# Kernel tuning notes

Measured on AMD Instinct MI355X. Metric: run time of the kernel, lower is better.

Reference implementation:

```python
import jax, jax.numpy as jnp
import numpy as np

T, B, NN = 20, 4, 500            # timesteps, batch, nodes per sample
M = B * NN                        # big-batched node count = 2000
IN_D, H, H2, OUT = 2, 128, 64, 32


def setup_inputs() -> dict:
    key = jax.random.key(0)
    ks = jax.random.split(key, 16)
    positions = jax.random.normal(ks[0], (T, M, IN_D), jnp.float32)
    adjacency = (jax.random.uniform(ks[1], (T, M, M)) < 0.01).astype(jnp.float32)
    adjacency = adjacency * (1.0 - jnp.eye(M, dtype=jnp.float32))
    ego_mask = jax.random.bernoulli(ks[2], 0.8, (B, T, NN))
    s = lambda k, shp, fan: (jax.random.normal(k, shp, jnp.float32) / np.sqrt(fan)).astype(jnp.float32)
    return {
        'positions': positions,
        'adjacency': adjacency,
        'ego_mask': ego_mask,
        'W1': s(ks[3], (IN_D, H), IN_D), 'b1': jnp.zeros((H,), jnp.float32),
        'W2': s(ks[4], (H, H), H),       'b2': jnp.zeros((H,), jnp.float32),
        'W_ih': s(ks[5], (4 * H, H), H), 'W_hh': s(ks[6], (4 * H, H), H),
        'b_ih': jnp.zeros((4 * H,), jnp.float32), 'b_hh': jnp.zeros((4 * H,), jnp.float32),
        'fc1_w': s(ks[7], (H, H2), H),   'fc1_b': jnp.zeros((H2,), jnp.float32),
        'fc2_w': s(ks[8], (H2, OUT), H2), 'fc2_b': jnp.zeros((OUT,), jnp.float32),
    }


def _forward(positions, adjacency, ego_mask, W1, b1, W2, b2,
             W_ih, W_hh, b_ih, b_hh, fc1_w, fc1_b, fc2_w, fc2_b):
    # ego_mask [B,T,NN] -> [T, B*NN] (matches permute(1,0,2).reshape(T,-1))
    mask = jnp.transpose(ego_mask, (1, 0, 2)).reshape(T, M).astype(positions.dtype)

    def gcn_timestep(x_t, a_t, m_t):
        # masked subgraph + self loops on kept nodes (PyG GCNConv normalization)
        Ahat = a_t * m_t[:, None] * m_t[None, :] + jnp.diag(m_t)   # [M,M]
        deg = Ahat.sum(axis=0)                                      # in-degree (col sum)
        dinv = jnp.where(deg > 0, jax.lax.rsqrt(jnp.maximum(deg, 1e-12)), 0.0)
        An = dinv[:, None] * Ahat * dinv[None, :]                   # D^-1/2 Ahat D^-1/2
        h1 = jax.nn.relu(An.T @ (x_t @ W1) + b1)                    # GCN1 + relu
        h2 = (An.T @ (h1 @ W2) + b2) * m_t[:, None]                 # GCN2, scatter into zeros
        return h2

    placeholder = jax.vmap(gcn_timestep)(positions, adjacency, mask)  # [T, M, H]

    # torch nn.LSTM (batch_first=False) on placeholder.transpose(0,1):
    # sequence axis = nodes (M), batch axis = T
    xs = jnp.transpose(placeholder, (1, 0, 2))  # [M, T, H]

    def lstm_step(carry, x_s):
        h, c = carry
        gates = x_s @ W_ih.T + b_ih + h @ W_hh.T + b_hh
        i, f, g, o = jnp.split(gates, 4, axis=-1)
        c = jax.nn.sigmoid(f) * c + jax.nn.sigmoid(i) * jnp.tanh(g)
        h = jax.nn.sigmoid(o) * jnp.tanh(c)
        return (h, c), h

    init = (jnp.zeros((T, H), positions.dtype), jnp.zeros((T, H), positions.dtype))
    _, lstm_out = jax.lax.scan(lstm_step, init, xs)  # [M, T, H]

    emb = lstm_out.reshape(B, NN, T, H)              # view(B, max_nodes, T, H)
    emb = jax.nn.relu(emb @ fc1_w + fc1_b)
    return emb @ fc2_w + fc2_b                       # [B, NN, T, OUT]


def reference(positions, adjacency, ego_mask, W1, b1, W2, b2,
              W_ih, W_hh, b_ih, b_hh, fc1_w, fc1_b, fc2_w, fc2_b):
    return _forward(positions, adjacency, ego_mask, W1, b1, W2, b2,
                    W_ih, W_hh, b_ih, b_hh, fc1_w, fc1_b, fc2_w, fc2_b)
```

## Files before the change

### kernel.cpp

```cpp
#include <hip/hip_runtime.h>
#include <hip/hip_bf16.h>

#define T_   20
#define B_   4
#define NN_  500
#define M_   2000
#define TM_  40000
#define H_   128
#define G_   512
#define H2_  64
#define OUT_ 32
#define ECAP 64
#define TG_  (T_ * G_)

typedef unsigned short ushort_t;
typedef unsigned int   uint_t;
typedef _Float16       f16;
typedef f16 f16x2 __attribute__((ext_vector_type(2)));

#if defined(__has_builtin)
#  if __has_builtin(__builtin_amdgcn_fdot2)
#    define HAVE_FDOT2 1
#  endif
#endif

__device__ inline float fdot2_(f16x2 a, f16x2 b, float c) {
#ifdef HAVE_FDOT2
    return __builtin_amdgcn_fdot2(a, b, c, false);
#else
    return c + (float)a.x * (float)b.x + (float)a.y * (float)b.y;
#endif
}

__device__ inline float fast_sig(float x) {
    float e = __builtin_amdgcn_exp2f(x * -1.4426950408889634f);
    return __builtin_amdgcn_rcpf(1.f + e);
}
__device__ inline float fast_tanh(float x) {
    float e = __builtin_amdgcn_exp2f(x * 2.8853900817779268f);
    return 1.f - 2.f * __builtin_amdgcn_rcpf(e + 1.f);
}

#define BARRAW() asm volatile("s_barrier" ::: "memory")

__global__ __launch_bounds__(1024) void k0_mask(const void* __restrict__ ego,
                                                float* __restrict__ mf,
                                                int* __restrict__ ecnt) {
    __shared__ int fl[3];
    int tid = threadIdx.x;
    if (tid < 3) fl[tid] = 0;
    __syncthreads();
    const uint_t* dw = (const uint_t*)ego;
    int a = 0, b = 0, c = 0;
    for (int i = tid; i < 2500; i += 1024) {
        uint_t v = dw[i];
        bool isf32  = (v == 0x3F800000u);
        bool isbf16 = (v == 0x00003F80u) || (v == 0x3F803F80u);
        if (isf32)  a = 1;
        if (isbf16) b = 1;
        if (v > 1u && !isf32 && !isbf16) c = 1;
    }
    if (a) fl[0] = 1;
    if (b) fl[1] = 1;
    if (c) fl[2] = 1;
    __syncthreads();
    int mode;
    if (fl[1])      mode = 3;
    else if (fl[0]) mode = 2;
    else if (fl[2]) mode = 1;
    else            mode = 0;
    int e = blockIdx.x * 1024 + tid;
    if (e >= TM_) return;
    ecnt[e] = 0;
    int t = e / M_, i = e % M_;
    int bb = i / NN_, n = i % NN_;
    int src = (bb * T_ + t) * NN_ + n;
    bool on;
    if (mode == 0)      on = ((const int*)ego)[src] != 0;
    else if (mode == 1) on = ((const unsigned char*)ego)[src] != 0;
    else if (mode == 2) on = ((const float*)ego)[src] != 0.f;
    else                on = ((const ushort_t*)ego)[src] != 0;
    mf[e] = on ? 1.f : 0.f;
}

#define JSTRIP 400
__global__ void k1_scan(const float* __restrict__ adj, const float* __restrict__ mf,
                        int* __restrict__ ecnt, int* __restrict__ edges) {
    __shared__ float ms[JSTRIP];
    int t = blockIdx.y, j0 = blockIdx.z * JSTRIP;
    int i = blockIdx.x * 256 + threadIdx.x;
    for (int idx = threadIdx.x; idx < JSTRIP; idx += 256)
        ms[idx] = mf[t * M_ + j0 + idx];
    __syncthreads();
    if (i >= M_) return;
    if (mf[t * M_ + i] == 0.f) return;
    const float* ap = adj + (size_t)t * M_ * M_ + (size_t)j0 * M_ + i;
    int r = t * M_ + i;
    int* ep = edges + (size_t)r * ECAP;
#pragma unroll 8
    for (int jj = 0; jj < JSTRIP; ++jj) {
        float av = ap[(size_t)jj * M_];
        if (av != 0.f && ms[jj] != 0.f) {
            int pos = atomicAdd(&ecnt[r], 1);
            if (pos < ECAP) ep[pos] = j0 + jj;
        }
    }
}

__global__ void k2_y1(const float* __restrict__ pos, const float* __restrict__ W1,
                      const float* __restrict__ mf, const int* __restrict__ ecnt,
                      float* __restrict__ dinv, f16* __restrict__ Y1) {
    int gid = blockIdx.x * 256 + threadIdx.x;
    int r = gid >> 7, h = gid & 127;
    if (r >= TM_) return;
    float mr = mf[r];
    int cnt = ecnt[r];
    float dv = (mr != 0.f) ? __frsqrt_rn((float)(cnt + 1)) : 0.f;
    if (h == 0) dinv[r] = dv;
    float2 xy = ((const float2*)pos)[r];
    float v = xy.x * W1[h] + xy.y * W1[H_ + h];
    Y1[gid] = (f16)(dv * v);
}

__global__ __launch_bounds__(64) void k3_agg1(const f16* __restrict__ Y1,
        const float* __restrict__ dinv, const int* __restrict__ ecnt,
        const int* __restrict__ edges, const float* __restrict__ b1,
        f16* __restrict__ h1) {
    int r = blockIdx.x, q = threadIdx.x;
    int t = r / M_, base = t * M_;
    const uint_t* Yu = (const uint_t*)Y1;
    f16x2 sp = __builtin_bit_cast(f16x2, Yu[(size_t)r * 64 + q]);
    float a0 = (float)sp.x, a1 = (float)sp.y;
    int ec = ecnt[r]; if (ec > ECAP) ec = ECAP;
    const int4* ep4 = (const int4*)(edges + (size_t)r * ECAP);
    for (int e = 0; e < ec; e += 4) {
        int4 ix = ep4[e >> 2];
        int j1 = (e + 1 < ec) ? ix.y : ix.x;
        int j2 = (e + 2 < ec) ? ix.z : ix.x;
        int j3 = (e + 3 < ec) ? ix.w : ix.x;
        uint_t u0 = Yu[(size_t)(base + ix.x) * 64 + q];
        uint_t u1 = Yu[(size_t)(base + j1) * 64 + q];
        uint_t u2 = Yu[(size_t)(base + j2) * 64 + q];
        uint_t u3 = Yu[(size_t)(base + j3) * 64 + q];
        f16x2 p0 = __builtin_bit_cast(f16x2, u0);
        a0 += (float)p0.x; a1 += (float)p0.y;
        if (e + 1 < ec) { f16x2 p = __builtin_bit_cast(f16x2, u1); a0 += (float)p.x; a1 += (float)p.y; }
        if (e + 2 < ec) { f16x2 p = __builtin_bit_cast(f16x2, u2); a0 += (float)p.x; a1 += (float)p.y; }
        if (e + 3 < ec) { f16x2 p = __builtin_bit_cast(f16x2, u3); a0 += (float)p.x; a1 += (float)p.y; }
    }
    float dv = dinv[r];
    float o0 = dv * a0 + b1[2 * q];
    float o1 = dv * a1 + b1[2 * q + 1];
    f16x2 op; op.x = (f16)fmaxf(o0, 0.f); op.y = (f16)fmaxf(o1, 0.f);
    ((uint_t*)h1)[(size_t)r * 64 + q] = __builtin_bit_cast(uint_t, op);
}

__global__ __launch_bounds__(64) void k5_agg2(const f16* __restrict__ Y2,
        const float* __restrict__ dinv, const float* __restrict__ mf,
        const int* __restrict__ ecnt, const int* __restrict__ edges,
        const float* __restrict__ b2, f16* __restrict__ ph) {
    int r = blockIdx.x, q = threadIdx.x;
    int t = r / M_, base = t * M_;
    const uint_t* Yu = (const uint_t*)Y2;
    f16x2 sp = __builtin_bit_cast(f16x2, Yu[(size_t)r * 64 + q]);
    float a0 = (float)sp.x, a1 = (float)sp.y;
    int ec = ecnt[r]; if (ec > ECAP) ec = ECAP;
    const int4* ep4 = (const int4*)(edges + (size_t)r * ECAP);
    for (int e = 0; e < ec; e += 4) {
        int4 ix = ep4[e >> 2];
        int j1 = (e + 1 < ec) ? ix.y : ix.x;
        int j2 = (e + 2 < ec) ? ix.z : ix.x;
        int j3 = (e + 3 < ec) ? ix.w : ix.x;
        uint_t u0 = Yu[(size_t)(base + ix.x) * 64 + q];
        uint_t u1 = Yu[(size_t)(base + j1) * 64 + q];
        uint_t u2 = Yu[(size_t)(base + j2) * 64 + q];
        uint_t u3 = Yu[(size_t)(base + j3) * 64 + q];
        f16x2 p0 = __builtin_bit_cast(f16x2, u0);
        a0 += (float)p0.x; a1 += (float)p0.y;
        if (e + 1 < ec) { f16x2 p = __builtin_bit_cast(f16x2, u1); a0 += (float)p.x; a1 += (float)p.y; }
        if (e + 2 < ec) { f16x2 p = __builtin_bit_cast(f16x2, u2); a0 += (float)p.x; a1 += (float)p.y; }
        if (e + 3 < ec) { f16x2 p = __builtin_bit_cast(f16x2, u3); a0 += (float)p.x; a1 += (float)p.y; }
    }
    float dv = dinv[r], mr = mf[r];
    f16x2 op;
    op.x = (f16)((dv * a0 + b2[2 * q]) * mr);
    op.y = (f16)((dv * a1 + b2[2 * q + 1]) * mr);
    ((uint_t*)ph)[(size_t)r * 64 + q] = __builtin_bit_cast(uint_t, op);
}

#define BM 32
#define BN 64
#define BLD (BN + 4)
__global__ __launch_bounds__(256) void kgemm(const f16* __restrict__ A,
        const float* __restrict__ Bw, int bTrans, int Ntot, int mode,
        const float* __restrict__ dinv, const float* __restrict__ ba,
        const float* __restrict__ bb, f16* __restrict__ Out) {
    __shared__ float As[H_ * BM];
    __shared__ float Bs[H_ * BLD];
    int m0 = blockIdx.x * BM;
    int nb = blockIdx.y;
    int tid = threadIdx.x;
    {
        int r = tid >> 3, kc = tid & 7;
        const f16* aprow = A + (size_t)(m0 + r) * H_ + kc * 16;
        float4 raw0 = ((const float4*)aprow)[0];
        float4 raw1 = ((const float4*)aprow)[1];
        f16 tmp[16];
        *(float4*)(tmp) = raw0;
        *(float4*)(tmp + 8) = raw1;
#pragma unroll
        for (int u = 0; u < 16; ++u) As[(kc * 16 + u) * BM + r] = (float)tmp[u];
    }
    if (bTrans == 0) {
        for (int idx = tid; idx < H_ * BN; idx += 256) {
            int k = idx >> 6, nl = idx & 63;
            Bs[k * BLD + nl] = Bw[k * Ntot + nb * BN + nl];
        }
    } else {
        for (int idx = tid; idx < H_ * BN; idx += 256) {
            int nl = idx >> 7, k = idx & 127;
            Bs[k * BLD + nl] = Bw[(size_t)(nb * BN + nl) * H_ + k];
        }
    }
    __syncthreads();
    int ty = tid >> 4, tx = tid & 15;
    float acc[2][4] = {};
#pragma unroll 4
    for (int k = 0; k < H_; ++k) {
        float2 a2 = *(const float2*)&As[k * BM + ty * 2];
        float4 b4 = *(const float4*)&Bs[k * BLD + tx * 4];
        acc[0][0] += a2.x * b4.x; acc[0][1] += a2.x * b4.y;
        acc[0][2] += a2.x * b4.z; acc[0][3] += a2.x * b4.w;
        acc[1][0] += a2.y * b4.x; acc[1][1] += a2.y * b4.y;
        acc[1][2] += a2.y * b4.z; acc[1][3] += a2.y * b4.w;
    }
#pragma unroll
    for (int rr = 0; rr < 2; ++rr) {
        int r = m0 + ty * 2 + rr;
        if (mode == 0) {
            float sc = dinv[r];
#pragma unroll
            for (int cc = 0; cc < 4; ++cc) {
                int n = nb * BN + tx * 4 + cc;
                Out[(size_t)r * Ntot + n] = (f16)(sc * acc[rr][cc]);
            }
        } else {
            int t = r / M_, s = r % M_;
#pragma unroll
            for (int cc = 0; cc < 4; ++cc) {
                int n = nb * BN + tx * 4 + cc;
                Out[((size_t)s * T_ + t) * G_ + n] =
                    (f16)(acc[rr][cc] + ba[n] + bb[n]);
            }
        }
    }
}

__global__ __launch_bounds__(512, 2) void k7_lstm(const float* __restrict__ Whh,
        const f16* __restrict__ xg, f16* __restrict__ lo) {
    __shared__ uint_t hbuf[H_ / 2];
    __shared__ float g4[G_];
    int t = blockIdx.x, j = threadIdx.x;
    f16x2 w[64];
    {
        const float* wr = Whh + (size_t)j * H_;
#pragma unroll
        for (int d = 0; d < 64; ++d) {
            f16x2 p;
            p.x = (f16)wr[2 * d];
            p.y = (f16)wr[2 * d + 1];
            w[d] = p;
        }
    }
    if (j < H_ / 2) hbuf[j] = 0;
    float cst = 0.f;
    const ushort_t* xpu = (const ushort_t*)xg + t * G_ + j;
    ushort_t xa[8], xb[8];
#pragma unroll
    for (int k = 0; k < 8; ++k) xa[k] = xpu[(size_t)k * TG_];
    __syncthreads();

#define LSTM_STEP(S, XV)                                                      \
    do {                                                                      \
        float acc = 0.f;                                                      \
        const uint4* hb = (const uint4*)hbuf;                                 \
        _Pragma("unroll")                                                     \
        for (int d = 0; d < 16; ++d) {                                        \
            uint4 hv = hb[d];                                                 \
            acc = fdot2_(w[4 * d + 0], __builtin_bit_cast(f16x2, hv.x), acc); \
            acc = fdot2_(w[4 * d + 1], __builtin_bit_cast(f16x2, hv.y), acc); \
            acc = fdot2_(w[4 * d + 2], __builtin_bit_cast(f16x2, hv.z), acc); \
            acc = fdot2_(w[4 * d + 3], __builtin_bit_cast(f16x2, hv.w), acc); \
        }                                                                     \
        acc += (float)__builtin_bit_cast(f16, (ushort_t)(XV));                \
        g4[j] = ((j >> 7) == 2) ? fast_tanh(acc) : fast_sig(acc);             \
        BARRAW();                                                             \
        if (j < H_) {                                                         \
            float si = g4[j], sf = g4[H_ + j];                                \
            float tg = g4[2 * H_ + j], so = g4[3 * H_ + j];                   \
            cst = sf * cst + si * tg;                                         \
            float h = so * fast_tanh(cst);                                    \
            f16 hh = (f16)h;                                                  \
            ((ushort_t*)hbuf)[j] = __builtin_bit_cast(ushort_t, hh);          \
            lo[((size_t)(S) * T_ + t) * H_ + j] = hh;                         \
        }                                                                     \
        BARRAW();                                                             \
    } while (0)

    for (int c2 = 0; c2 < 125; ++c2) {
        int sA = c2 * 16;
#pragma unroll
        for (int k = 0; k < 8; ++k) xb[k] = xpu[(size_t)(sA + 8 + k) * TG_];
#pragma unroll
        for (int k = 0; k < 8; ++k) LSTM_STEP(sA + k, xa[k]);
        int nbs = (sA + 16 <= TM_ / T_ - 8) ? sA + 16 : TM_ / T_ - 8;
#pragma unroll
        for (int k = 0; k < 8; ++k) xa[k] = xpu[(size_t)(nbs + k) * TG_];
#pragma unroll
        for (int k = 0; k < 8; ++k) LSTM_STEP(sA + 8 + k, xb[k]);
    }
#undef LSTM_STEP
}

__global__ __launch_bounds__(256) void k8_fc(const f16* __restrict__ lo,
        const float* __restrict__ w1, const float* __restrict__ fb1,
        const float* __restrict__ w2, const float* __restrict__ fb2,
        float* __restrict__ out) {
    __shared__ uint_t hl[4][H_ / 2];
    __shared__ float o1f[4][H2_];
    int tid = threadIdx.x;
    int o = tid & 63, rr = tid >> 6;
    f16x2 w1c[64];
#pragma unroll
    for (int d = 0; d < 64; ++d) {
        f16x2 p;
        p.x = (f16)w1[(2 * d) * H2_ + o];
        p.y = (f16)w1[(2 * d + 1) * H2_ + o];
        w1c[d] = p;
    }
    int o2 = o & 31;
    float w2f[64];
#pragma unroll
    for (int d = 0; d < 64; ++d) w2f[d] = w2[d * OUT_ + o2];
    float fb1v = fb1[o], fb2v = fb2[o2];

    for (int r0 = blockIdx.x * 4; r0 < TM_; r0 += 512 * 4) {
        {
            int row = tid >> 6, q = tid & 63;
            hl[row][q] = ((const uint_t*)lo)[(size_t)(r0 + row) * 64 + q];
        }
        __syncthreads();
        float acc = fb1v;
        const uint4* hb = (const uint4*)&hl[rr][0];
#pragma unroll
        for (int d = 0; d < 16; ++d) {
            uint4 hv = hb[d];
            acc = fdot2_(w1c[4 * d + 0], __builtin_bit_cast(f16x2, hv.x), acc);
            acc = fdot2_(w1c[4 * d + 1], __builtin_bit_cast(f16x2, hv.y), acc);
            acc = fdot2_(w1c[4 * d + 2], __builtin_bit_cast(f16x2, hv.z), acc);
            acc = fdot2_(w1c[4 * d + 3], __builtin_bit_cast(f16x2, hv.w), acc);
        }
        o1f[rr][o] = fmaxf(acc, 0.f);
        __syncthreads();
        if (o < OUT_) {
            float a2 = fb2v;
            const float4* ob = (const float4*)&o1f[rr][0];
#pragma unroll
            for (int d = 0; d < 16; ++d) {
                float4 v = ob[d];
                a2 += v.x * w2f[4 * d + 0] + v.y * w2f[4 * d + 1]
                    + v.z * w2f[4 * d + 2] + v.w * w2f[4 * d + 3];
            }
            out[(size_t)(r0 + rr) * OUT_ + o] = a2;
        }
        __syncthreads();
    }
}

extern "C" void kernel_launch(void* const* d_in, const int* in_sizes, int n_in,
                              void* d_out, int out_size, void* d_ws, size_t ws_size,
                              hipStream_t stream) {
    const float* positions = (const float*)d_in[0];
    const float* adjacency = (const float*)d_in[1];
    const void*  ego       = d_in[2];
    const float* W1   = (const float*)d_in[3];
    const float* b1   = (const float*)d_in[4];
    const float* W2   = (const float*)d_in[5];
    const float* b2   = (const float*)d_in[6];
    const float* W_ih = (const float*)d_in[7];
    const float* W_hh = (const float*)d_in[8];
    const float* b_ih = (const float*)d_in[9];
    const float* b_hh = (const float*)d_in[10];
    const float* fc1w = (const float*)d_in[11];
    const float* fc1b = (const float*)d_in[12];
    const float* fc2w = (const float*)d_in[13];
    const float* fc2b = (const float*)d_in[14];
    float* out = (float*)d_out;

    char* p = (char*)d_ws;
    auto alloc = [&](size_t bytes) {
        void* r = (void*)p;
        p += (bytes + 255) & ~(size_t)255;
        return r;
    };
    float* mf    = (float*)alloc((size_t)TM_ * 4);
    float* dinv  = (float*)alloc((size_t)TM_ * 4);
    int*   ecnt  = (int*)alloc((size_t)TM_ * 4);
    int*   edges = (int*)alloc((size_t)TM_ * ECAP * 4);
    f16*   bufC  = (f16*)alloc((size_t)TM_ * H_ * 2);
    f16*   bufD  = (f16*)alloc((size_t)TM_ * H_ * 2);
    f16*   xg    = (f16*)alloc((size_t)TM_ * G_ * 2);
    f16*   Y1 = bufC, *Y2 = bufC;
    f16*   h1 = bufD, *ph = bufD;
    f16*   lo = (f16*)edges;

    hipLaunchKernelGGL(k0_mask, dim3(40), dim3(1024), 0, stream, ego, mf, ecnt);
    hipLaunchKernelGGL(k1_scan, dim3(8, 20, 5), dim3(256), 0, stream,
                       adjacency, mf, ecnt, edges);
    hipLaunchKernelGGL(k2_y1, dim3(20000), dim3(256), 0, stream,
                       positions, W1, mf, ecnt, dinv, Y1);
    hipLaunchKernelGGL(k3_agg1, dim3(40000), dim3(64), 0, stream,
                       Y1, dinv, ecnt, edges, b1, h1);
    hipLaunchKernelGGL(kgemm, dim3(1250, 2), dim3(256), 0, stream,
                       h1, W2, 0, 128, 0, dinv, (const float*)nullptr,
                       (const float*)nullptr, Y2);
    hipLaunchKernelGGL(k5_agg2, dim3(40000), dim3(64), 0, stream,
                       Y2, dinv, mf, ecnt, edges, b2, ph);
    hipLaunchKernelGGL(kgemm, dim3(1250, 8), dim3(256), 0, stream,
                       ph, W_ih, 1, 512, 1, dinv, b_ih, b_hh, xg);
    hipLaunchKernelGGL(k7_lstm, dim3(20), dim3(512), 0, stream, W_hh, xg, lo);
    hipLaunchKernelGGL(k8_fc, dim3(512), dim3(256), 0, stream,
                       lo, fc1w, fc1b, fc2w, fc2b, out);
}
```

Before: 1.914 ms.

## Use MFMA for dense GEMMs, restructure LSTM step, and split adjacency scan finer

The fp32 FMA GEMM is replaced by an f16 MFMA kernel with 64x64 tiles in LDS. The LSTM kernel is reorganised so each group of four threads computes all four gates for one hidden unit, reduced with lane shuffles. This removes the gate shared-memory array and one barrier per step, and double-buffers the hidden state. The adjacency scan strip is halved to launch more blocks. The LSTM is a long serial chain, so cutting its per-step barriers and latency is likely the main target. The shuffle reductions add latency to each step in exchange.

Result: no change. 1.918 ms (+0.2%).

```diff
diff --git a/kernel.cpp b/kernel.cpp
--- a/kernel.cpp
+++ b/kernel.cpp
@@ -17,6 +17,8 @@
 typedef unsigned int   uint_t;
 typedef _Float16       f16;
 typedef f16 f16x2 __attribute__((ext_vector_type(2)));
+typedef f16 f16x8 __attribute__((ext_vector_type(8)));
+typedef float f32x4 __attribute__((ext_vector_type(4)));
 
 #if defined(__has_builtin)
 #  if __has_builtin(__builtin_amdgcn_fdot2)
@@ -83,7 +85,7 @@
     mf[e] = on ? 1.f : 0.f;
 }
 
-#define JSTRIP 400
+#define JSTRIP 200
 __global__ void k1_scan(const float* __restrict__ adj, const float* __restrict__ mf,
                         int* __restrict__ ecnt, int* __restrict__ edges) {
     __shared__ float ms[JSTRIP];
@@ -188,69 +190,80 @@
     ((uint_t*)ph)[(size_t)r * 64 + q] = __builtin_bit_cast(uint_t, op);
 }
 
-#define BM 32
-#define BN 64
-#define BLD (BN + 4)
-__global__ __launch_bounds__(256) void kgemm(const f16* __restrict__ A,
+#define ALD 136
+__global__ __launch_bounds__(256) void kgemm_mfma(const f16* __restrict__ A,
         const float* __restrict__ Bw, int bTrans, int Ntot, int mode,
         const float* __restrict__ dinv, const float* __restrict__ ba,
         const float* __restrict__ bb, f16* __restrict__ Out) {
-    __shared__ float As[H_ * BM];
-    __shared__ float Bs[H_ * BLD];
-    int m0 = blockIdx.x * BM;
-    int nb = blockIdx.y;
+    __shared__ f16 As[64 * ALD];
+    __shared__ f16 Bs[64 * ALD];
+    int m0 = blockIdx.x * 64;
+    int n0 = blockIdx.y * 64;
     int tid = threadIdx.x;
-    {
-        int r = tid >> 3, kc = tid & 7;
-        const f16* aprow = A + (size_t)(m0 + r) * H_ + kc * 16;
-        float4 raw0 = ((const float4*)aprow)[0];
-        float4 raw1 = ((const float4*)aprow)[1];
-        f16 tmp[16];
-        *(float4*)(tmp) = raw0;
-        *(float4*)(tmp + 8) = raw1;
-#pragma unroll
-        for (int u = 0; u < 16; ++u) As[(kc * 16 + u) * BM + r] = (float)tmp[u];
-    }
-    if (bTrans == 0) {
-        for (int idx = tid; idx < H_ * BN; idx += 256) {
-            int k = idx >> 6, nl = idx & 63;
-            Bs[k * BLD + nl] = Bw[k * Ntot + nb * BN + nl];
+#pragma unroll
+    for (int u = 0; u < 4; ++u) {
+        int idx = u * 256 + tid;
+        int row = idx >> 4, seg = idx & 15;
+        *(f16x8*)&As[row * ALD + seg * 8] =
+            *(const f16x8*)(A + (size_t)(m0 + row) * H_ + seg * 8);
+    }
+    if (bTrans) {
+#pragma unroll
+        for (int u = 0; u < 16; ++u) {
+            int idx = u * 256 + tid;
+            int n = idx >> 6, k2 = (idx & 63) * 2;
+            float2 v = *(const float2*)(Bw + (size_t)(n0 + n) * H_ + k2);
+            f16x2 pk; pk.x = (f16)v.x; pk.y = (f16)v.y;
+            *(uint_t*)&Bs[n * ALD + k2] = __builtin_bit_cast(uint_t, pk);
         }
     } else {
-        for (int idx = tid; idx < H_ * BN; idx += 256) {
-            int nl = idx >> 7, k = idx & 127;
-            Bs[k * BLD + nl] = Bw[(size_t)(nb * BN + nl) * H_ + k];
+#pragma unroll
+        for (int u = 0; u < 16; ++u) {
+            int idx = u * 256 + tid;
+            int n = idx >> 6, k2 = (idx & 63) * 2;
+            f16x2 pk;
+            pk.x = (f16)Bw[(size_t)k2 * Ntot + n0 + n];
+            pk.y = (f16)Bw[(size_t)(k2 + 1) * Ntot + n0 + n];
+            *(uint_t*)&Bs[n * ALD + k2] = __builtin_bit_cast(uint_t, pk);
         }
     }
     __syncthreads();
-    int ty = tid >> 4, tx = tid & 15;
-    float acc[2][4] = {};
-#pragma unroll 4
-    for (int k = 0; k < H_; ++k) {
-        float2 a2 = *(const float2*)&As[k * BM + ty * 2];
-        float4 b4 = *(const float4*)&Bs[k * BLD + tx * 4];
-        acc[0][0] += a2.x * b4.x; acc[0][1] += a2.x * b4.y;
-        acc[0][2] += a2.x * b4.z; acc[0][3] += a2.x * b4.w;
-        acc[1][0] += a2.y * b4.x; acc[1][1] += a2.y * b4.y;
-        acc[1][2] += a2.y * b4.z; acc[1][3] += a2.y * b4.w;
-    }
-#pragma unroll
-    for (int rr = 0; rr < 2; ++rr) {
-        int r = m0 + ty * 2 + rr;
-        if (mode == 0) {
-            float sc = dinv[r];
-#pragma unroll
-            for (int cc = 0; cc < 4; ++cc) {
-                int n = nb * BN + tx * 4 + cc;
-                Out[(size_t)r * Ntot + n] = (f16)(sc * acc[rr][cc]);
+    int w = tid >> 6, lane = tid & 63;
+    int col = lane & 15, quad = lane >> 4;
+    f32x4 acc[4] = {};
+#pragma unroll
+    for (int kk = 0; kk < 4; ++kk) {
+        f16x8 af = *(const f16x8*)&As[(w * 16 + col) * ALD + kk * 32 + quad * 8];
+#pragma unroll
+        for (int nt = 0; nt < 4; ++nt) {
+            f16x8 bf = *(const f16x8*)&Bs[(nt * 16 + col) * ALD + kk * 32 + quad * 8];
+            acc[nt] = __builtin_amdgcn_mfma_f32_16x16x32_f16(af, bf, acc[nt], 0, 0, 0);
+        }
+    }
+    if (mode == 0) {
+        float dv[4];
+#pragma unroll
+        for (int reg = 0; reg < 4; ++reg)
+            dv[reg] = dinv[m0 + w * 16 + quad * 4 + reg];
+#pragma unroll
+        for (int nt = 0; nt < 4; ++nt) {
+            int n = n0 + nt * 16 + col;
+#pragma unroll
+            for (int reg = 0; reg < 4; ++reg) {
+                int r = m0 + w * 16 + quad * 4 + reg;
+                Out[(size_t)r * Ntot + n] = (f16)(dv[reg] * acc[nt][reg]);
             }
-        } else {
-            int t = r / M_, s = r % M_;
-#pragma unroll
-            for (int cc = 0; cc < 4; ++cc) {
-                int n = nb * BN + tx * 4 + cc;
-                Out[((size_t)s * T_ + t) * G_ + n] =
-                    (f16)(acc[rr][cc] + ba[n] + bb[n]);
+        }
+    } else {
+#pragma unroll
+        for (int nt = 0; nt < 4; ++nt) {
+            int n = n0 + nt * 16 + col;
+            float bias = ba[n] + bb[n];
+#pragma unroll
+            for (int reg = 0; reg < 4; ++reg) {
+                int r = m0 + w * 16 + quad * 4 + reg;
+                int t = r / M_, s = r % M_;
+                Out[((size_t)s * T_ + t) * G_ + n] = (f16)(acc[nt][reg] + bias);
             }
         }
     }
@@ -258,23 +271,32 @@
 
 __global__ __launch_bounds__(512, 2) void k7_lstm(const float* __restrict__ Whh,
         const f16* __restrict__ xg, f16* __restrict__ lo) {
-    __shared__ uint_t hbuf[H_ / 2];
-    __shared__ float g4[G_];
-    int t = blockIdx.x, j = threadIdx.x;
-    f16x2 w[64];
+    __shared__ uint_t hb2[2][H_ / 2];
+    int t = blockIdx.x, tid = threadIdx.x;
+    int h = tid >> 2, q = tid & 3;
+    f16x2 w0[16], w1[16], w2[16], w3[16];
     {
-        const float* wr = Whh + (size_t)j * H_;
-#pragma unroll
-        for (int d = 0; d < 64; ++d) {
+        const float* base = Whh + (size_t)h * H_ + q * 32;
+#pragma unroll
+        for (int d = 0; d < 16; ++d) {
             f16x2 p;
-            p.x = (f16)wr[2 * d];
-            p.y = (f16)wr[2 * d + 1];
-            w[d] = p;
-        }
-    }
-    if (j < H_ / 2) hbuf[j] = 0;
+            p.x = (f16)base[0 * G_ * 32 + 2 * d];
+            p.y = (f16)base[0 * G_ * 32 + 2 * d + 1];
+            w0[d] = p;
+            p.x = (f16)base[(size_t)H_ * H_ + 2 * d];
+            p.y = (f16)base[(size_t)H_ * H_ + 2 * d + 1];
+            w1[d] = p;
+            p.x = (f16)base[(size_t)2 * H_ * H_ + 2 * d];
+            p.y = (f16)base[(size_t)2 * H_ * H_ + 2 * d + 1];
+            w2[d] = p;
+            p.x = (f16)base[(size_t)3 * H_ * H_ + 2 * d];
+            p.y = (f16)base[(size_t)3 * H_ * H_ + 2 * d + 1];
+            w3[d] = p;
+        }
+    }
+    if (tid < H_ / 2) hb2[0][tid] = 0;
     float cst = 0.f;
-    const ushort_t* xpu = (const ushort_t*)xg + t * G_ + j;
+    const ushort_t* xpu = (const ushort_t*)xg + t * G_ + q * H_ + h;
     ushort_t xa[8], xb[8];
 #pragma unroll
     for (int k = 0; k < 8; ++k) xa[k] = xpu[(size_t)k * TG_];
@@ -282,27 +304,42 @@
 
 #define LSTM_STEP(S, XV)                                                      \
     do {                                                                      \
-        float acc = 0.f;                                                      \
-        const uint4* hb = (const uint4*)hbuf;                                 \
+        const uint4* hbp = (const uint4*)&hb2[(S) & 1][0];                    \
+        float a0 = 0.f, a1 = 0.f, a2 = 0.f, a3 = 0.f;                         \
         _Pragma("unroll")                                                     \
-        for (int d = 0; d < 16; ++d) {                                        \
-            uint4 hv = hb[d];                                                 \
-            acc = fdot2_(w[4 * d + 0], __builtin_bit_cast(f16x2, hv.x), acc); \
-            acc = fdot2_(w[4 * d + 1], __builtin_bit_cast(f16x2, hv.y), acc); \
-            acc = fdot2_(w[4 * d + 2], __builtin_bit_cast(f16x2, hv.z), acc); \
-            acc = fdot2_(w[4 * d + 3], __builtin_bit_cast(f16x2, hv.w), acc); \
+        for (int d = 0; d < 4; ++d) {                                         \
+            uint4 hv = hbp[q * 4 + d];                                        \
+            f16x2 e0 = __builtin_bit_cast(f16x2, hv.x);                       \
+            f16x2 e1 = __builtin_bit_cast(f16x2, hv.y);                       \
+            f16x2 e2 = __builtin_bit_cast(f16x2, hv.z);                       \
+            f16x2 e3 = __builtin_bit_cast(f16x2, hv.w);                       \
+            a0 = fdot2_(w0[4 * d + 3], e3, fdot2_(w0[4 * d + 2], e2,          \
+                 fdot2_(w0[4 * d + 1], e1, fdot2_(w0[4 * d + 0], e0, a0))));  \
+            a1 = fdot2_(w1[4 * d + 3], e3, fdot2_(w1[4 * d + 2], e2,          \
+                 fdot2_(w1[4 * d + 1], e1, fdot2_(w1[4 * d + 0], e0, a1))));  \
+            a2 = fdot2_(w2[4 * d + 3], e3, fdot2_(w2[4 * d + 2], e2,          \
+                 fdot2_(w2[4 * d + 1], e1, fdot2_(w2[4 * d + 0], e0, a2))));  \
+            a3 = fdot2_(w3[4 * d + 3], e3, fdot2_(w3[4 * d + 2], e2,          \
+                 fdot2_(w3[4 * d + 1], e1, fdot2_(w3[4 * d + 0], e0, a3))));  \
         }                                                                     \
-        acc += (float)__builtin_bit_cast(f16, (ushort_t)(XV));                \
-        g4[j] = ((j >> 7) == 2) ? fast_tanh(acc) : fast_sig(acc);             \
-        BARRAW();                                                             \
-        if (j < H_) {                                                         \
-            float si = g4[j], sf = g4[H_ + j];                                \
-            float tg = g4[2 * H_ + j], so = g4[3 * H_ + j];                   \
-            cst = sf * cst + si * tg;                                         \
-            float h = so * fast_tanh(cst);                                    \
-            f16 hh = (f16)h;                                                  \
-            ((ushort_t*)hbuf)[j] = __builtin_bit_cast(ushort_t, hh);          \
-            lo[((size_t)(S) * T_ + t) * H_ + j] = hh;                         \
+        float xf = (float)__builtin_bit_cast(f16, (ushort_t)(XV));            \
+        a0 += (q == 0) ? xf : 0.f;                                            \
+        a1 += (q == 1) ? xf : 0.f;                                            \
+        a2 += (q == 2) ? xf : 0.f;                                            \
+        a3 += (q == 3) ? xf : 0.f;                                            \
+        a0 += __shfl_xor(a0, 1); a0 += __shfl_xor(a0, 2);                     \
+        a1 += __shfl_xor(a1, 1); a1 += __shfl_xor(a1, 2);                     \
+        a2 += __shfl_xor(a2, 1); a2 += __shfl_xor(a2, 2);                     \
+        a3 += __shfl_xor(a3, 1); a3 += __shfl_xor(a3, 2);                     \
+        float gi = fast_sig(a0), gf = fast_sig(a1);                           \
+        float gg = fast_tanh(a2), go = fast_sig(a3);                          \
+        cst = gf * cst + gi * gg;                                             \
+        float hv_ = go * fast_tanh(cst);                                      \
+        if (q == 0) {                                                         \
+            f16 hh = (f16)hv_;                                                \
+            ((ushort_t*)&hb2[((S) & 1) ^ 1][0])[h] =                          \
+                __builtin_bit_cast(ushort_t, hh);                             \
+            lo[((size_t)(S) * T_ + t) * H_ + h] = hh;                         \
         }                                                                     \
         BARRAW();                                                             \
     } while (0)
@@ -313,7 +350,7 @@
         for (int k = 0; k < 8; ++k) xb[k] = xpu[(size_t)(sA + 8 + k) * TG_];
 #pragma unroll
         for (int k = 0; k < 8; ++k) LSTM_STEP(sA + k, xa[k]);
-        int nbs = (sA + 16 <= TM_ / T_ - 8) ? sA + 16 : TM_ / T_ - 8;
+        int nbs = (sA + 16 <= M_ - 8) ? sA + 16 : M_ - 8;
 #pragma unroll
         for (int k = 0; k < 8; ++k) xa[k] = xpu[(size_t)(nbs + k) * TG_];
 #pragma unroll
@@ -346,8 +383,8 @@
 
     for (int r0 = blockIdx.x * 4; r0 < TM_; r0 += 512 * 4) {
         {
-            int row = tid >> 6, q = tid & 63;
-            hl[row][q] = ((const uint_t*)lo)[(size_t)(r0 + row) * 64 + q];
+            int row = tid >> 6, qq = tid & 63;
+            hl[row][qq] = ((const uint_t*)lo)[(size_t)(r0 + row) * 64 + qq];
         }
         __syncthreads();
         float acc = fb1v;
@@ -415,18 +452,18 @@
     f16*   lo = (f16*)edges;
 
     hipLaunchKernelGGL(k0_mask, dim3(40), dim3(1024), 0, stream, ego, mf, ecnt);
-    hipLaunchKernelGGL(k1_scan, dim3(8, 20, 5), dim3(256), 0, stream,
+    hipLaunchKernelGGL(k1_scan, dim3(8, 20, 10), dim3(256), 0, stream,
                        adjacency, mf, ecnt, edges);
     hipLaunchKernelGGL(k2_y1, dim3(20000), dim3(256), 0, stream,
                        positions, W1, mf, ecnt, dinv, Y1);
     hipLaunchKernelGGL(k3_agg1, dim3(40000), dim3(64), 0, stream,
                        Y1, dinv, ecnt, edges, b1, h1);
-    hipLaunchKernelGGL(kgemm, dim3(1250, 2), dim3(256), 0, stream,
+    hipLaunchKernelGGL(kgemm_mfma, dim3(625, 2), dim3(256), 0, stream,
                        h1, W2, 0, 128, 0, dinv, (const float*)nullptr,
                        (const float*)nullptr, Y2);
     hipLaunchKernelGGL(k5_agg2, dim3(40000), dim3(64), 0, stream,
                        Y2, dinv, mf, ecnt, edges, b2, ph);
-    hipLaunchKernelGGL(kgemm, dim3(1250, 8), dim3(256), 0, stream,
+    hipLaunchKernelGGL(kgemm_mfma, dim3(625, 8), dim3(256), 0, stream,
                        ph, W_ih, 1, 512, 1, dinv, b_ih, b_hh, xg);
     hipLaunchKernelGGL(k7_lstm, dim3(20), dim3(512), 0, stream, W_hh, xg, lo);
     hipLaunchKernelGGL(k8_fc, dim3(512), dim3(256), 0, stream,
```
